# Kernel tuning notes

Measured on AMD Instinct MI355X. Metric: run time of the kernel, lower is better.

Reference implementation:

```python
import jax, jax.numpy as jnp
import numpy as np

DIM = 1024
CTX_DIM = 1024
HEADS = 16
DIM_HEAD = 64
INNER = HEADS * DIM_HEAD  # 1024
FF_INNER = 4 * DIM        # 4096
EPS = 1e-5


def layer_norm(x, g, b):
    mu = jnp.mean(x, axis=-1, keepdims=True)
    var = jnp.var(x, axis=-1, keepdims=True)
    return (x - mu) * jax.lax.rsqrt(var + EPS) * g + b


def setup_inputs() -> dict:
    key = jax.random.key(0)
    ks = jax.random.split(key, 9)
    b, n, j = 4, 2048, 1024
    inp = {
        "x": jax.random.normal(ks[0], (b, n, DIM), dtype=jnp.float32),
        "context": jax.random.normal(ks[1], (b, j, CTX_DIM), dtype=jnp.float32),
        "ln_g": jnp.ones((DIM,), jnp.float32),
        "ln_b": jnp.zeros((DIM,), jnp.float32),
        "cln_g": jnp.ones((CTX_DIM,), jnp.float32),
        "cln_b": jnp.zeros((CTX_DIM,), jnp.float32),
        "Wq": jax.random.normal(ks[2], (DIM, INNER), dtype=jnp.float32) * (DIM ** -0.5),
        "Wkv": jax.random.normal(ks[3], (CTX_DIM, 2 * DIM_HEAD), dtype=jnp.float32) * (CTX_DIM ** -0.5),
        "Wo": jax.random.normal(ks[4], (INNER, DIM), dtype=jnp.float32) * (INNER ** -0.5),
        "Wff1": jax.random.normal(ks[5], (DIM, 2 * FF_INNER), dtype=jnp.float32) * (DIM ** -0.5),
        "Wff2": jax.random.normal(ks[6], (FF_INNER, DIM), dtype=jnp.float32) * (FF_INNER ** -0.5),
    }
    return inp


def reference(x, context, ln_g, ln_b, cln_g, cln_b, Wq, Wkv, Wo, Wff1, Wff2):
    scale = DIM_HEAD ** -0.5
    xn = layer_norm(x, ln_g, ln_b)                       # [b, n, dim]
    cn = layer_norm(context, cln_g, cln_b)               # [b, j, ctx_dim]
    b, n, _ = xn.shape
    q = (xn @ Wq).reshape(b, n, HEADS, DIM_HEAD).transpose(0, 2, 1, 3) * scale  # [b,h,n,d]
    kv = cn @ Wkv                                        # [b, j, 2d]
    k, v = kv[..., :DIM_HEAD], kv[..., DIM_HEAD:]        # [b, j, d] each (shared head)
    sim = jnp.einsum('bhid,bjd->bhij', q, k)
    attn = jax.nn.softmax(sim, axis=-1)
    out = jnp.einsum('bhij,bjd->bhid', attn, v)          # [b,h,n,d]
    out = out.transpose(0, 2, 1, 3).reshape(b, n, INNER) @ Wo  # [b,n,dim]
    # parallel SwiGLU FF on normed x
    ff = xn @ Wff1                                       # [b,n,2*ff_inner]
    h, gate = ff[..., :FF_INNER], ff[..., FF_INNER:]
    out = out + (jax.nn.silu(gate) * h) @ Wff2
    return out
```

## Files before the change

kernel.cpp:

```cpp
#include <hip/hip_runtime.h>
#include <math.h>

typedef unsigned short u16;
typedef __attribute__((ext_vector_type(8))) short short8;
typedef __attribute__((ext_vector_type(8))) unsigned short ushortx8;
typedef __attribute__((ext_vector_type(4))) unsigned short ushortx4;
typedef __attribute__((ext_vector_type(4))) float floatx4;

#define DEVI __device__ __forceinline__

DEVI float bf2f(u16 u) {
    unsigned int i = ((unsigned int)u) << 16;
    float f; __builtin_memcpy(&f, &i, 4); return f;
}
DEVI u16 f2bf(float f) {
    unsigned int i; __builtin_memcpy(&i, &f, 4);
    i += 0x7fffu + ((i >> 16) & 1u);
    return (u16)(i >> 16);
}
DEVI void gl_lds16(const void* g, void* l) {
    __builtin_amdgcn_global_load_lds(
        (const __attribute__((address_space(1))) void*)g,
        (__attribute__((address_space(3))) void*)l, 16, 0, 0);
}

template <bool FF1>
__global__ void transpose_kernel(const float* __restrict__ B, u16* __restrict__ BT,
                                 int K, int N) {
    __shared__ u16 t[32][33];
    int nb = blockIdx.x * 32, kb = blockIdx.y * 32;
    int tx = threadIdx.x, ty = threadIdx.y;
    for (int i = ty; i < 32; i += 8)
        t[i][tx] = f2bf(B[(size_t)(kb + i) * N + nb + tx]);
    __syncthreads();
    for (int i = ty; i < 32; i += 8) {
        int c = nb + i;
        int r_out = FF1 ? ((((c & 4095) >> 4) << 5) + ((c >> 12) << 4) + (c & 15)) : c;
        BT[(size_t)r_out * K + kb + tx] = t[tx][i];
    }
}

__global__ __launch_bounds__(256)
void ln_kernel(const float* __restrict__ x, const float* __restrict__ g,
               const float* __restrict__ b, u16* __restrict__ out) {
    __shared__ float sw[4], sw2[4];
    const int tid = threadIdx.x, wave = tid >> 6, lane = tid & 63;
    const float* xr = x + (size_t)blockIdx.x * 1024;
    float4 v = *(const float4*)(xr + tid * 4);
    float f[4] = {v.x, v.y, v.z, v.w};
    float s = f[0] + f[1] + f[2] + f[3];
    float s2 = f[0]*f[0] + f[1]*f[1] + f[2]*f[2] + f[3]*f[3];
    for (int o = 32; o; o >>= 1) {
        s  += __shfl_xor(s,  o, 64);
        s2 += __shfl_xor(s2, o, 64);
    }
    if (lane == 0) { sw[wave] = s; sw2[wave] = s2; }
    __syncthreads();
    float tot  = sw[0] + sw[1] + sw[2] + sw[3];
    float tot2 = sw2[0] + sw2[1] + sw2[2] + sw2[3];
    float mu  = tot * (1.f / 1024.f);
    float var = tot2 * (1.f / 1024.f) - mu * mu;
    float rs  = rsqrtf(var + 1e-5f);
    float4 gv = *(const float4*)(g + tid * 4);
    float4 bv = *(const float4*)(b + tid * 4);
    ushortx4 ov;
    ov[0] = f2bf((f[0] - mu) * rs * gv.x + bv.x);
    ov[1] = f2bf((f[1] - mu) * rs * gv.y + bv.y);
    ov[2] = f2bf((f[2] - mu) * rs * gv.z + bv.z);
    ov[3] = f2bf((f[3] - mu) * rs * gv.w + bv.w);
    *(ushortx4*)(out + (size_t)blockIdx.x * 1024 + tid * 4) = ov;
}

enum { EPI_PLAIN = 0, EPI_Q = 1, EPI_KV = 2, EPI_ADD_F32 = 3 };

template <int EPI>
__global__ __launch_bounds__(256)
void gemm_bt_kernel(const u16* __restrict__ A, const u16* __restrict__ BT,
                    void* __restrict__ Cv, u16* __restrict__ AUX,
                    int M, int N, int K) {
    __shared__ u16 As[128 * 32];
    __shared__ u16 Bs[128 * 32];
    const int tid = threadIdx.x, wave = tid >> 6, lane = tid & 63;
    const int mbase = blockIdx.x * 128, nbase = blockIdx.y * 128;
    const int m0 = (wave & 1) * 64, n0 = (wave >> 1) * 64;
    const int lrow = lane & 15, lq = lane >> 4;

    floatx4 zero = {0.f, 0.f, 0.f, 0.f};
    floatx4 acc[4][4];
#pragma unroll
    for (int i = 0; i < 4; i++)
#pragma unroll
        for (int j = 0; j < 4; j++) acc[i][j] = zero;

    for (int kt = 0; kt < K; kt += 32) {
#pragma unroll
        for (int i = 0; i < 2; i++) {
            int e = i * 2048 + tid * 8;
            int r = e >> 5, c = e & 31;
            gl_lds16(A  + (size_t)(mbase + r) * K + kt + c, As + e);
            gl_lds16(BT + (size_t)(nbase + r) * K + kt + c, Bs + e);
        }
        __syncthreads();
        short8 af[4], bf[4];
#pragma unroll
        for (int f = 0; f < 4; f++) {
            af[f] = *(const short8*)(As + (m0 + f * 16 + lrow) * 32 + lq * 8);
            bf[f] = *(const short8*)(Bs + (n0 + f * 16 + lrow) * 32 + lq * 8);
        }
#pragma unroll
        for (int i = 0; i < 4; i++)
#pragma unroll
            for (int j = 0; j < 4; j++)
                acc[i][j] = __builtin_amdgcn_mfma_f32_16x16x32_bf16(af[i], bf[j], acc[i][j], 0, 0, 0);
        __syncthreads();
    }

#pragma unroll
    for (int mf = 0; mf < 4; mf++)
#pragma unroll
        for (int nf = 0; nf < 4; nf++)
#pragma unroll
            for (int r = 0; r < 4; r++) {
                int row = mbase + m0 + mf * 16 + lq * 4 + r;
                int col = nbase + n0 + nf * 16 + lrow;
                float v = acc[mf][nf][r];
                if constexpr (EPI == EPI_PLAIN) {
                    ((u16*)Cv)[(size_t)row * N + col] = f2bf(v);
                } else if constexpr (EPI == EPI_Q) {
                    int b = row >> 11, i2 = row & 2047, h = col >> 6, d = col & 63;
                    ((u16*)Cv)[((size_t)((b * 16 + h) * 2048 + i2)) * 64 + d] = f2bf(v * 0.125f);
                } else if constexpr (EPI == EPI_KV) {
                    int b = row >> 10, j = row & 1023;
                    if (col < 64) ((u16*)Cv)[(size_t)row * 64 + col] = f2bf(v);
                    else AUX[((size_t)(b * 64 + (col - 64))) * 1024 + j] = f2bf(v);
                } else {
                    ((float*)Cv)[(size_t)row * N + col] = v + bf2f(AUX[(size_t)row * N + col]);
                }
            }
}

__global__ __launch_bounds__(512, 2)
void gemm256_ff1_kernel(const u16* __restrict__ A, const u16* __restrict__ BT,
                        u16* __restrict__ C, int K) {
    extern __shared__ float4 smem4[];
    char* smem = (char*)smem4;

    const int tid = threadIdx.x, wave = tid >> 6, lane = tid & 63;
    const int wm = wave >> 2, wn = wave & 3;
    const int lrow = lane & 15, lq = lane >> 4;

    const int bid = blockIdx.x;
    const int xcd = bid & 7, s = bid >> 3;
    const int mbase = (s >> 2) * 256;
    const int nbase = (xcd * 4 + (s & 3)) * 256;

    const int sl = (tid & 7) ^ ((tid >> 3) & 7);
    const u16* aBase = A  + (size_t)(mbase + (tid >> 3)) * K + sl * 8;
    const u16* bBase = BT + (size_t)(nbase + (tid >> 3)) * K + sl * 8;
    char* dst0 = smem + tid * 16;

#define STAGE_A(buf_, h_, kt_) do {                                        \
        char* d_ = dst0 + (buf_) * 65536 + (h_) * 16384;                   \
        gl_lds16(aBase + (size_t)(h_) * 128 * K + (kt_), d_);              \
        gl_lds16(aBase + (size_t)((h_) * 128 + 64) * K + (kt_), d_ + 8192);\
    } while (0)
#define STAGE_B(buf_, h_, kt_) do {                                        \
        char* d_ = dst0 + 32768 + (buf_) * 65536 + (h_) * 16384;           \
        gl_lds16(bBase + (size_t)(h_) * 128 * K + (kt_), d_);              \
        gl_lds16(bBase + (size_t)((h_) * 128 + 64) * K + (kt_), d_ + 8192);\
    } while (0)
#define BAR() do { asm volatile("" ::: "memory");                          \
        __builtin_amdgcn_s_barrier();                                      \
        asm volatile("" ::: "memory"); } while (0)
#define MFMA16(Q, AF, BF) do {                                             \
        __builtin_amdgcn_s_setprio(1);                                     \
        _Pragma("unroll") for (int mf_ = 0; mf_ < 4; ++mf_)                \
        _Pragma("unroll") for (int nf_ = 0; nf_ < 2; ++nf_)                \
        _Pragma("unroll") for (int ks_ = 0; ks_ < 2; ++ks_)                \
            acc[Q][mf_][nf_] = __builtin_amdgcn_mfma_f32_16x16x32_bf16(    \
                AF[mf_][ks_], BF[nf_][ks_], acc[Q][mf_][nf_], 0, 0, 0);    \
        __builtin_amdgcn_s_setprio(0); } while (0)

    floatx4 zero = {0.f, 0.f, 0.f, 0.f};
    floatx4 acc[4][4][2];
#pragma unroll
    for (int q = 0; q < 4; ++q)
#pragma unroll
        for (int i = 0; i < 4; ++i)
#pragma unroll
            for (int j = 0; j < 2; ++j) acc[q][i][j] = zero;

    const int cb0 = ((0 + lq) ^ (lrow & 7)) << 4;
    const int cb1 = ((4 + lq) ^ (lrow & 7)) << 4;

    const int NT = K >> 6;

    STAGE_A(0, 0, 0); STAGE_B(0, 0, 0); STAGE_A(0, 1, 0); STAGE_B(0, 1, 0);
    STAGE_A(1, 0, 64); STAGE_B(1, 0, 64);
    asm volatile("s_waitcnt vmcnt(4)" ::: "memory");
    BAR();

    for (int t = 0; t < NT; ++t) {
        const int bu = t & 1;
        const char* Ab = smem + bu * 65536 + (size_t)((wm * 64 + lrow) * 128);
        const char* Bb = smem + bu * 65536 + 32768 + (size_t)((wn * 32 + lrow) * 128);

        if (t + 1 < NT) { STAGE_A(bu ^ 1, 1, (t + 1) * 64); STAGE_B(bu ^ 1, 1, (t + 1) * 64); }

        short8 af[4][2], a2[4][2], bf0[2][2], bf1[2][2];
#pragma unroll
        for (int mf = 0; mf < 4; ++mf) {
            af[mf][0] = *(const short8*)(Ab + mf * 2048 + cb0);
            af[mf][1] = *(const short8*)(Ab + mf * 2048 + cb1);
        }
#pragma unroll
        for (int nf = 0; nf < 2; ++nf) {
            bf0[nf][0] = *(const short8*)(Bb + nf * 2048 + cb0);
            bf0[nf][1] = *(const short8*)(Bb + nf * 2048 + cb1);
            bf1[nf][0] = *(const short8*)(Bb + 16384 + nf * 2048 + cb0);
            bf1[nf][1] = *(const short8*)(Bb + 16384 + nf * 2048 + cb1);
        }
#pragma unroll
        for (int mf = 0; mf < 4; ++mf) {
            a2[mf][0] = *(const short8*)(Ab + 16384 + mf * 2048 + cb0);
            a2[mf][1] = *(const short8*)(Ab + 16384 + mf * 2048 + cb1);
        }

        MFMA16(0, af, bf0);
        MFMA16(1, af, bf1);
        BAR();
        if (t + 2 < NT) { STAGE_A(bu, 0, (t + 2) * 64); STAGE_B(bu, 0, (t + 2) * 64); }
        MFMA16(2, a2, bf0);
        MFMA16(3, a2, bf1);

        if (t + 2 < NT) asm volatile("s_waitcnt vmcnt(4)" ::: "memory");
        else            asm volatile("s_waitcnt vmcnt(0)" ::: "memory");
        BAR();
    }
#undef STAGE_A
#undef STAGE_B
#undef BAR
#undef MFMA16

    const int orow = mbase + wm * 64 + lq * 4;
    const int og16 = (nbase >> 5) + wn;
#pragma unroll
    for (int q = 0; q < 4; ++q) {
        const int qm = q >> 1, qn = q & 1;
#pragma unroll
        for (int mf = 0; mf < 4; ++mf)
#pragma unroll
            for (int r = 0; r < 4; ++r) {
                float hv = acc[q][mf][0][r], gv = acc[q][mf][1][r];
                float act = hv * (gv / (1.f + __expf(-gv)));
                int row = orow + qm * 128 + mf * 16 + r;
                int col = (og16 + qn * 4) * 16 + lrow;
                C[(size_t)row * 4096 + col] = f2bf(act);
            }
    }
}

__global__ __launch_bounds__(256)
void attn_kernel(const u16* __restrict__ q, const u16* __restrict__ k,
                 const u16* __restrict__ vt, u16* __restrict__ o) {
    __shared__ char smem[53248];
    u16* Qs  = (u16*)smem;
    u16* Ps  = (u16*)smem;
    u16* Ks  = (u16*)(smem + 17408);
    u16* VTs = (u16*)(smem + 35840);
    float* Lp   = (float*)(smem + 17408);
    float* Ltot = (float*)(smem + 18432);

    const int tid = threadIdx.x, wave = tid >> 6, lane = tid & 63;
    const int lrow = lane & 15, lq = lane >> 4;
    const int b = blockIdx.z, h = blockIdx.y, mt = blockIdx.x;

    const u16* qb = q + ((size_t)((b * 16 + h) * 2048) + mt * 64) * 64;
    const u16* kb = k + (size_t)b * 1024 * 64;
    const u16* vb = vt + (size_t)b * 64 * 1024;

#pragma unroll
    for (int i = 0; i < 2; i++) {
        int e = i * 2048 + tid * 8;
        int r = e >> 6, d = e & 63;
        *(ushortx8*)(Qs + r * 72 + d) = *(const ushortx8*)(qb + e);
    }
    __syncthreads();
    short8 qf[2][4];
#pragma unroll
    for (int ks = 0; ks < 2; ks++)
#pragma unroll
        for (int cf = 0; cf < 4; cf++)
            qf[ks][cf] = *(const short8*)(Qs + (cf * 16 + lrow) * 72 + ks * 32 + lq * 8);

    floatx4 zero = {0.f, 0.f, 0.f, 0.f};
    floatx4 oacc[4];
#pragma unroll
    for (int i = 0; i < 4; i++) oacc[i] = zero;
    float lsum[4] = {0.f, 0.f, 0.f, 0.f};

    for (int jt = 0; jt < 8; jt++) {
#pragma unroll
        for (int i = 0; i < 4; i++) {
            int e = i * 2048 + tid * 8;
            int r = e >> 6, d = e & 63;
            *(ushortx8*)(Ks + r * 72 + d) = *(const ushortx8*)(kb + jt * 8192 + e);
            int dv = e >> 7, jj = e & 127;
            *(ushortx8*)(VTs + dv * 136 + jj) =
                *(const ushortx8*)(vb + (size_t)dv * 1024 + jt * 128 + jj);
        }
        __syncthreads();

        floatx4 sacc[2][4];
#pragma unroll
        for (int rf = 0; rf < 2; rf++)
#pragma unroll
            for (int cf = 0; cf < 4; cf++) sacc[rf][cf] = zero;
#pragma unroll
        for (int ks = 0; ks < 2; ks++) {
            short8 af[2];
#pragma unroll
            for (int rf = 0; rf < 2; rf++)
                af[rf] = *(const short8*)(Ks + (wave * 32 + rf * 16 + lrow) * 72 + ks * 32 + lq * 8);
#pragma unroll
            for (int rf = 0; rf < 2; rf++)
#pragma unroll
                for (int cf = 0; cf < 4; cf++)
                    sacc[rf][cf] = __builtin_amdgcn_mfma_f32_16x16x32_bf16(af[rf], qf[ks][cf], sacc[rf][cf], 0, 0, 0);
        }

#pragma unroll
        for (int rf = 0; rf < 2; rf++)
#pragma unroll
            for (int cf = 0; cf < 4; cf++) {
                float p0 = __expf(sacc[rf][cf][0]);
                float p1 = __expf(sacc[rf][cf][1]);
                float p2 = __expf(sacc[rf][cf][2]);
                float p3 = __expf(sacc[rf][cf][3]);
                lsum[cf] += p0 + p1 + p2 + p3;
                ushortx4 pk = {f2bf(p0), f2bf(p1), f2bf(p2), f2bf(p3)};
                int m = cf * 16 + lrow;
                int j0 = wave * 32 + rf * 16 + lq * 4;
                *(ushortx4*)(Ps + m * 136 + j0) = pk;
            }
        __syncthreads();

#pragma unroll
        for (int ks = 0; ks < 4; ks++) {
            short8 pf[4];
#pragma unroll
            for (int mf = 0; mf < 4; mf++)
                pf[mf] = *(const short8*)(Ps + (mf * 16 + lrow) * 136 + ks * 32 + lq * 8);
            short8 vf = *(const short8*)(VTs + (wave * 16 + lrow) * 136 + ks * 32 + lq * 8);
#pragma unroll
            for (int mf = 0; mf < 4; mf++)
                oacc[mf] = __builtin_amdgcn_mfma_f32_16x16x32_bf16(pf[mf], vf, oacc[mf], 0, 0, 0);
        }
        __syncthreads();
    }

    float lv[4];
#pragma unroll
    for (int cf = 0; cf < 4; cf++) {
        float v = lsum[cf];
        v += __shfl_xor(v, 16, 64);
        v += __shfl_xor(v, 32, 64);
        lv[cf] = v;
    }
    if (lane < 16) {
#pragma unroll
        for (int cf = 0; cf < 4; cf++) Lp[wave * 64 + cf * 16 + lane] = lv[cf];
    }
    __syncthreads();
    if (tid < 64) Ltot[tid] = Lp[tid] + Lp[64 + tid] + Lp[128 + tid] + Lp[192 + tid];
    __syncthreads();

    const int d = wave * 16 + lrow;
    const size_t orow0 = (size_t)(b * 2048 + mt * 64);
#pragma unroll
    for (int mf = 0; mf < 4; mf++)
#pragma unroll
        for (int r = 0; r < 4; r++) {
            int m = mf * 16 + lq * 4 + r;
            float val = oacc[mf][r] / Ltot[m];
            o[(orow0 + m) * 1024 + h * 64 + d] = f2bf(val);
        }
}

extern "C" void kernel_launch(void* const* d_in, const int* in_sizes, int n_in,
                              void* d_out, int out_size, void* d_ws, size_t ws_size,
                              hipStream_t stream) {
    const float* x     = (const float*)d_in[0];
    const float* ctx   = (const float*)d_in[1];
    const float* ln_g  = (const float*)d_in[2];
    const float* ln_b  = (const float*)d_in[3];
    const float* cln_g = (const float*)d_in[4];
    const float* cln_b = (const float*)d_in[5];
    const float* Wq    = (const float*)d_in[6];
    const float* Wkv   = (const float*)d_in[7];
    const float* Wo    = (const float*)d_in[8];
    const float* Wff1  = (const float*)d_in[9];
    const float* Wff2  = (const float*)d_in[10];
    (void)in_sizes; (void)n_in; (void)out_size; (void)ws_size;

    u16* ws = (u16*)d_ws;
    const size_t MiB = 524288;
    u16* ffa   = ws;
    u16* qb    = ws;
    u16* attnb = ws + 16 * MiB;
    u16* cn    = ws + 32 * MiB;
    u16* kb    = ws + 40 * MiB;
    u16* vtb   = ws + 40 * MiB + 262144;
    u16* WqT   = ws + 41 * MiB;
    u16* WkvT  = ws + 43 * MiB;
    u16* WoT   = ws + 44 * MiB;
    u16* xn    = ws + 64 * MiB;
    u16* wo    = ws + 80 * MiB;
    u16* Wff1T = ws + 96 * MiB;
    u16* Wff2T = ws + 112 * MiB;

    static bool attr_set = false;
    if (!attr_set) {
        hipFuncSetAttribute(reinterpret_cast<const void*>(gemm256_ff1_kernel),
                            hipFuncAttributeMaxDynamicSharedMemorySize, 131072);
        attr_set = true;
    }

    dim3 tb(32, 8);
    transpose_kernel<false><<<dim3(32, 32),  tb, 0, stream>>>(Wq,   WqT,   1024, 1024);
    transpose_kernel<false><<<dim3(4, 32),   tb, 0, stream>>>(Wkv,  WkvT,  1024, 128);
    transpose_kernel<false><<<dim3(32, 32),  tb, 0, stream>>>(Wo,   WoT,   1024, 1024);
    transpose_kernel<true> <<<dim3(256, 32), tb, 0, stream>>>(Wff1, Wff1T, 1024, 8192);
    transpose_kernel<false><<<dim3(32, 128), tb, 0, stream>>>(Wff2, Wff2T, 4096, 1024);

    ln_kernel<<<8192, 256, 0, stream>>>(x,   ln_g,  ln_b,  xn);
    ln_kernel<<<4096, 256, 0, stream>>>(ctx, cln_g, cln_b, cn);

    gemm_bt_kernel<EPI_Q> <<<dim3(64, 8), 256, 0, stream>>>(xn, WqT,  qb, nullptr, 8192, 1024, 1024);
    gemm_bt_kernel<EPI_KV><<<dim3(32, 1), 256, 0, stream>>>(cn, WkvT, kb, vtb,     4096, 128,  1024);

    attn_kernel<<<dim3(32, 16, 4), 256, 0, stream>>>(qb, kb, vtb, attnb);

    gemm_bt_kernel<EPI_PLAIN><<<dim3(64, 8), 256, 0, stream>>>(attnb, WoT, wo, nullptr, 8192, 1024, 1024);
    gemm256_ff1_kernel<<<dim3(1024), 512, 131072, stream>>>(xn, Wff1T, ffa, 1024);
    gemm_bt_kernel<EPI_ADD_F32><<<dim3(64, 8), 256, 0, stream>>>(ffa, Wff2T, d_out, wo, 8192, 1024, 4096);
}
```

Baseline: 586.8 us.

## Prefetch next K/V tile into registers during attention compute and raise MFMA priority

The attention kernel now loads the next K and V^T tile from global memory into registers at the start of each iteration and writes it to LDS after the PV step. Global load latency can then overlap with the QK and PV MFMA work, where before every iteration stalled on the loads. s_setprio is also raised around the MFMA sections. This adds register pressure for 8 vector registers per thread and an extra barrier per iteration, which may lower occupancy.

```diff
diff --git a/kernel.cpp b/kernel.cpp
--- a/kernel.cpp
+++ b/kernel.cpp
@@ -279,12 +279,28 @@
     const u16* kb = k + (size_t)b * 1024 * 64;
     const u16* vb = vt + (size_t)b * 64 * 1024;
 
+    ushortx8 kreg[4], vreg[4];
+#define LOADJT(jt_) do { _Pragma("unroll") for (int i_ = 0; i_ < 4; ++i_) {   \
+        int e_ = i_ * 2048 + tid * 8;                                         \
+        kreg[i_] = *(const ushortx8*)(kb + (jt_) * 8192 + e_);                \
+        int dv_ = e_ >> 7, jj_ = e_ & 127;                                    \
+        vreg[i_] = *(const ushortx8*)(vb + (size_t)dv_ * 1024 + (jt_) * 128 + jj_); \
+    } } while (0)
+#define WRITEJT() do { _Pragma("unroll") for (int i_ = 0; i_ < 4; ++i_) {     \
+        int e_ = i_ * 2048 + tid * 8;                                         \
+        int r_ = e_ >> 6, d_ = e_ & 63;                                       \
+        *(ushortx8*)(Ks + r_ * 72 + d_) = kreg[i_];                           \
+        int dv_ = e_ >> 7, jj_ = e_ & 127;                                    \
+        *(ushortx8*)(VTs + dv_ * 136 + jj_) = vreg[i_];                       \
+    } } while (0)
+
 #pragma unroll
     for (int i = 0; i < 2; i++) {
         int e = i * 2048 + tid * 8;
         int r = e >> 6, d = e & 63;
         *(ushortx8*)(Qs + r * 72 + d) = *(const ushortx8*)(qb + e);
     }
+    LOADJT(0);
     __syncthreads();
     short8 qf[2][4];
 #pragma unroll
@@ -292,6 +308,8 @@
 #pragma unroll
         for (int cf = 0; cf < 4; cf++)
             qf[ks][cf] = *(const short8*)(Qs + (cf * 16 + lrow) * 72 + ks * 32 + lq * 8);
+    WRITEJT();
+    __syncthreads();
 
     floatx4 zero = {0.f, 0.f, 0.f, 0.f};
     floatx4 oacc[4];
@@ -300,22 +318,14 @@
     float lsum[4] = {0.f, 0.f, 0.f, 0.f};
 
     for (int jt = 0; jt < 8; jt++) {
-#pragma unroll
-        for (int i = 0; i < 4; i++) {
-            int e = i * 2048 + tid * 8;
-            int r = e >> 6, d = e & 63;
-            *(ushortx8*)(Ks + r * 72 + d) = *(const ushortx8*)(kb + jt * 8192 + e);
-            int dv = e >> 7, jj = e & 127;
-            *(ushortx8*)(VTs + dv * 136 + jj) =
-                *(const ushortx8*)(vb + (size_t)dv * 1024 + jt * 128 + jj);
-        }
-        __syncthreads();
+        if (jt + 1 < 8) LOADJT(jt + 1);
 
         floatx4 sacc[2][4];
 #pragma unroll
         for (int rf = 0; rf < 2; rf++)
 #pragma unroll
             for (int cf = 0; cf < 4; cf++) sacc[rf][cf] = zero;
+        __builtin_amdgcn_s_setprio(1);
 #pragma unroll
         for (int ks = 0; ks < 2; ks++) {
             short8 af[2];
@@ -328,6 +338,7 @@
                 for (int cf = 0; cf < 4; cf++)
                     sacc[rf][cf] = __builtin_amdgcn_mfma_f32_16x16x32_bf16(af[rf], qf[ks][cf], sacc[rf][cf], 0, 0, 0);
         }
+        __builtin_amdgcn_s_setprio(0);
 
 #pragma unroll
         for (int rf = 0; rf < 2; rf++)
@@ -345,6 +356,7 @@
             }
         __syncthreads();
 
+        __builtin_amdgcn_s_setprio(1);
 #pragma unroll
         for (int ks = 0; ks < 4; ks++) {
             short8 pf[4];
@@ -356,8 +368,16 @@
             for (int mf = 0; mf < 4; mf++)
                 oacc[mf] = __builtin_amdgcn_mfma_f32_16x16x32_bf16(pf[mf], vf, oacc[mf], 0, 0, 0);
         }
+        __builtin_amdgcn_s_setprio(0);
         __syncthreads();
-    }
+
+        if (jt + 1 < 8) {
+            WRITEJT();
+            __syncthreads();
+        }
+    }
+#undef LOADJT
+#undef WRITEJT
 
     float lv[4];
 #pragma unroll
```

Measured after the change: 566.1 us. 3.5% less time.
